# Performance work log

Hardware: AMD Instinct MI355X
Metric: run time of the kernel (lower is better)

## Reference

```python
import jax, jax.numpy as jnp
import numpy as np

EPS = 1e-8


def setup_inputs() -> dict:
    key = jax.random.key(0)
    k1, k2, k3, k4 = jax.random.split(key, 4)
    N, D, P, H = 8192, 512, 128, 128
    x1 = jax.random.normal(k1, (N, D), dtype=jnp.float32)
    proj_w1 = jax.random.normal(k2, (D, D), dtype=jnp.float32) * (1.0 / np.sqrt(D))
    proj_w2 = jax.random.normal(k3, (D, P), dtype=jnp.float32) * (1.0 / np.sqrt(D))
    gc_w = jax.random.normal(k4, (D, H), dtype=jnp.float32) * (1.0 / np.sqrt(D))
    gc_b = jnp.zeros((H,), dtype=jnp.float32)
    return {"x1": x1, "proj_w1": proj_w1, "proj_w2": proj_w2, "gc_w": gc_w, "gc_b": gc_b}


def _cosine_similarity(x):
    # torch.mm(x, x.T) / clamp(||x|| * ||x||.T, eps)
    w = jnp.sqrt(jnp.sum(x * x, axis=1, keepdims=True))  # [N,1]
    return (x @ x.T) / jnp.maximum(w * w.T, EPS)


def reference(x1, proj_w1, proj_w2, gc_w, gc_b):
    # projector: Linear(512,512,bias=False) -> ReLU -> Linear(512,P,bias=False)
    x_proj = jax.nn.relu(x1 @ proj_w1) @ proj_w2  # [N,P]
    # graph build is under @torch.no_grad(): dense fully-connected weighted graph
    A = jax.lax.stop_gradient(_cosine_similarity(x_proj))  # [N,N]
    N = x1.shape[0]
    # WGraphConv (DGL GraphConv w/ edge weights, norm='both'):
    # fully connected graph incl. self loops -> in_degree = N, norm = N^{-1/2} on both sides
    inv_n = jnp.asarray(1.0 / N, dtype=x1.dtype)
    h = x1 @ gc_w            # project first (D > H, cheaper)  [N,H]
    h = (A @ h) * inv_n      # weighted aggregate, symmetric degree norm
    return h + gc_b          # [N,H]
```

## Files before the change

### kernel.cpp

```cpp
#include <hip/hip_runtime.h>
#include <stdint.h>
#include <stddef.h>

typedef short s16x4 __attribute__((ext_vector_type(4)));
typedef short s16x8 __attribute__((ext_vector_type(8)));
typedef float f32x4 __attribute__((ext_vector_type(4)));

#define NN 8192
#define DD 512
#define PP 128
#define HH 128

__device__ __forceinline__ short f2bf(float f) {
  unsigned u = __builtin_bit_cast(unsigned, f);
  u = (u + 0x7fffu + ((u >> 16) & 1u)) >> 16;
  return (short)u;
}

__device__ __forceinline__ void async16(const void* g, void* l) {
  __builtin_amdgcn_global_load_lds(
      (const __attribute__((address_space(1))) unsigned int*)g,
      (__attribute__((address_space(3))) unsigned int*)l, 16, 0, 0);
}

template <int MF>
__device__ __forceinline__ void gemm_core2(
    const short* __restrict__ A, long lda,
    const short* __restrict__ BT, long ldb,
    long rowBase, long colBase, int k0, int k1,
    short* As0, short* Bs0, short* As1, short* Bs1,
    f32x4 (*acc)[4]) {
  const int tid  = threadIdx.x;
  const int lane = tid & 63;
  const int wid  = tid >> 6;
  const int wr   = (wid >> 1) * (MF * 16);
  const int wc   = (wid & 1) * 64;
  const int srow = lane >> 3;
  const int skk  = (lane & 7) * 8;

#define STAGE_(AS, BS, KK)                                                    \
  do {                                                                        \
    _Pragma("unroll")                                                         \
    for (int it = 0; it < MF; ++it) {                                         \
      int r = wid * (MF * 8) + it * 8;                                        \
      async16(A + (rowBase + r + srow) * lda + (KK) + skk, (AS) + r * 64);    \
    }                                                                         \
    _Pragma("unroll")                                                         \
    for (int it = 0; it < 4; ++it) {                                          \
      int r = wid * 32 + it * 8;                                              \
      async16(BT + (colBase + r + srow) * ldb + (KK) + skk, (BS) + r * 64);   \
    }                                                                         \
  } while (0)

  STAGE_(As0, Bs0, k0);
  __syncthreads();
  for (int k = k0; k < k1; k += 64) {
    if (k + 64 < k1) STAGE_(As1, Bs1, k + 64);
#pragma unroll
    for (int ks = 0; ks < 64; ks += 32) {
      s16x8 af[MF], bfv[4];
#pragma unroll
      for (int i = 0; i < MF; ++i)
        af[i]  = *(const s16x8*)(As0 + (wr + i * 16 + (lane & 15)) * 64 + ks + (lane >> 4) * 8);
#pragma unroll
      for (int i = 0; i < 4; ++i)
        bfv[i] = *(const s16x8*)(Bs0 + (wc + i * 16 + (lane & 15)) * 64 + ks + (lane >> 4) * 8);
#pragma unroll
      for (int mi = 0; mi < MF; ++mi)
#pragma unroll
        for (int ni = 0; ni < 4; ++ni)
          acc[mi][ni] = __builtin_amdgcn_mfma_f32_16x16x32_bf16(af[mi], bfv[ni], acc[mi][ni], 0, 0, 0);
    }
    __syncthreads();
    short* t0 = As0; As0 = As1; As1 = t0;
    short* t1 = Bs0; Bs0 = Bs1; Bs1 = t1;
  }
#undef STAGE_
}

__device__ __forceinline__ void zero_acc2(f32x4 (*acc)[4], int mf) {
  f32x4 z = {0.f, 0.f, 0.f, 0.f};
  for (int i = 0; i < mf; ++i)
    for (int j = 0; j < 4; ++j) acc[i][j] = z;
}

__global__ __launch_bounds__(256) void k_prep(
    const float* __restrict__ x1, const float* __restrict__ w1,
    const float* __restrict__ w2, const float* __restrict__ gcw,
    short* __restrict__ x1b, short* __restrict__ w1t,
    short* __restrict__ w2t, short* __restrict__ gcwt) {
  long b = blockIdx.x;
  int t = threadIdx.x;
  if (b < 4096) {
    long i = b * 256 + t;
    float4 v = ((const float4*)x1)[i];
    s16x4 o;
    o[0] = f2bf(v.x); o[1] = f2bf(v.y); o[2] = f2bf(v.z); o[3] = f2bf(v.w);
    *(s16x4*)(x1b + i * 4) = o;
  } else if (b < 4096 + 1024) {
    long i = (b - 4096) * 256 + t;
    int n = (int)(i >> 9), k = (int)(i & 511);
    w1t[i] = f2bf(w1[(long)k * DD + n]);
  } else if (b < 4096 + 1024 + 256) {
    long i = (b - 5120) * 256 + t;
    int n = (int)(i >> 9), k = (int)(i & 511);
    w2t[i] = f2bf(w2[(long)k * PP + n]);
  } else {
    long i = (b - 5376) * 256 + t;
    int n = (int)(i >> 9), k = (int)(i & 511);
    gcwt[i] = f2bf(gcw[(long)k * HH + n]);
  }
}

__global__ __launch_bounds__(256) void k_g13(const short* __restrict__ x1b,
                                             const short* __restrict__ w1t,
                                             const short* __restrict__ gcwt,
                                             short* __restrict__ Y,
                                             short* __restrict__ hT) {
  __shared__ __align__(16) char smem[49152];
  short* As0 = (short*)smem;
  short* As1 = (short*)(smem + 8192);
  short* Bs0 = (short*)(smem + 16384);
  short* Bs1 = (short*)(smem + 32768);
  f32x4 acc[2][4];
  zero_acc2(acc, 2);
  const int bx = blockIdx.x;
  const int lane = threadIdx.x & 63, wid = threadIdx.x >> 6;
  const int wr = (wid >> 1) * 32, wc = (wid & 1) * 64;
  if (bx < 512) {
    long rowBase = (long)(bx >> 2) * 64;
    long colBase = (long)(bx & 3) * 128;
    gemm_core2<2>(x1b, DD, w1t, DD, rowBase, colBase, 0, DD, As0, Bs0, As1, Bs1, acc);
#pragma unroll
    for (int mi = 0; mi < 2; ++mi)
#pragma unroll
      for (int ni = 0; ni < 4; ++ni)
#pragma unroll
        for (int r = 0; r < 4; ++r) {
          long m = rowBase + wr + mi * 16 + ((lane >> 4) << 2) + r;
          long n = colBase + wc + ni * 16 + (lane & 15);
          float v = acc[mi][ni][r];
          Y[m * DD + n] = f2bf(v > 0.f ? v : 0.f);
        }
  } else {
    long rowBase = (long)(bx - 512) * 64;
    gemm_core2<2>(x1b, DD, gcwt, DD, rowBase, 0, 0, DD, As0, Bs0, As1, Bs1, acc);
    short (*hs)[66] = (short(*)[66])smem;
#pragma unroll
    for (int mi = 0; mi < 2; ++mi)
#pragma unroll
      for (int ni = 0; ni < 4; ++ni)
#pragma unroll
        for (int r = 0; r < 4; ++r) {
          int m = wr + mi * 16 + ((lane >> 4) << 2) + r;
          int n = wc + ni * 16 + (lane & 15);
          hs[n][m] = f2bf(acc[mi][ni][r]);
        }
    __syncthreads();
    int t = threadIdx.x;
    int h = t >> 1, m0 = (t & 1) * 32;
#pragma unroll
    for (int j0 = 0; j0 < 32; j0 += 8) {
      s16x8 o;
#pragma unroll
      for (int u = 0; u < 8; ++u) o[u] = hs[h][m0 + j0 + u];
      *(s16x8*)(hT + (long)h * NN + rowBase + m0 + j0) = o;
    }
  }
}

__global__ __launch_bounds__(256) void k_g2(const short* __restrict__ Y,
                                            const short* __restrict__ w2t,
                                            short* __restrict__ xp,
                                            short* __restrict__ xpT,
                                            float* __restrict__ invnw) {
  __shared__ __align__(16) char smem[49152];
  short* As0 = (short*)smem;
  short* As1 = (short*)(smem + 8192);
  short* Bs0 = (short*)(smem + 16384);
  short* Bs1 = (short*)(smem + 32768);
  __shared__ float invw_s[64];
  f32x4 acc[2][4];
  zero_acc2(acc, 2);
  long rowBase = (long)blockIdx.x * 64;
  gemm_core2<2>(Y, DD, w2t, DD, rowBase, 0, 0, DD, As0, Bs0, As1, Bs1, acc);
  const int lane = threadIdx.x & 63, wid = threadIdx.x >> 6;
  const int wr = (wid >> 1) * 32, wc = (wid & 1) * 64;
  float (*xs)[129] = (float(*)[129])smem;
#pragma unroll
  for (int mi = 0; mi < 2; ++mi)
#pragma unroll
    for (int ni = 0; ni < 4; ++ni)
#pragma unroll
      for (int r = 0; r < 4; ++r)
        xs[wr + mi * 16 + ((lane >> 4) << 2) + r][wc + ni * 16 + (lane & 15)] = acc[mi][ni][r];
  __syncthreads();
  int t = threadIdx.x;
  if (t < 64) {
    float s = 0.f;
#pragma unroll 8
    for (int i = 0; i < 128; ++i) { int c = (t + i) & 127; float v = xs[t][c]; s += v * v; }
    float nr = sqrtf(s);
    invnw[rowBase + t] = 1.f / (8192.f * nr);
    invw_s[t] = 1.f / nr;
  }
  __syncthreads();
#pragma unroll
  for (int i = 0; i < 4; ++i) {
    int seg = i * 256 + t;
    int r = seg >> 4, c0 = (seg & 15) * 8;
    s16x8 o;
#pragma unroll
    for (int u = 0; u < 8; ++u) o[u] = f2bf(xs[r][c0 + u]);
    *(s16x8*)(xp + (long)(rowBase + r) * PP + c0) = o;
  }
  int c = t >> 1, n0 = (t & 1) * 32;
#pragma unroll
  for (int j0 = 0; j0 < 32; j0 += 8) {
    s16x8 o;
#pragma unroll
    for (int u = 0; u < 8; ++u) {
      int n = n0 + j0 + u;
      o[u] = f2bf(xs[n][c] * invw_s[n]);
    }
    *(s16x8*)(xpT + (long)c * NN + rowBase + n0 + j0) = o;
  }
}

__global__ __launch_bounds__(256) void k_ge(const short* __restrict__ xpT,
                                            const short* __restrict__ hT,
                                            float* __restrict__ Gp) {
  __shared__ __align__(16) char smem[65536];
  short* As0 = (short*)smem;
  short* As1 = (short*)(smem + 16384);
  short* Bs0 = (short*)(smem + 32768);
  short* Bs1 = (short*)(smem + 49152);
  f32x4 acc[4][4];
  zero_acc2(acc, 4);
  int s = blockIdx.x;
  gemm_core2<4>(xpT, NN, hT, NN, 0, 0, s * 128, s * 128 + 128, As0, Bs0, As1, Bs1, acc);
  const int lane = threadIdx.x & 63, wid = threadIdx.x >> 6;
  const int wr = (wid >> 1) * 64, wc = (wid & 1) * 64;
#pragma unroll
  for (int mi = 0; mi < 4; ++mi)
#pragma unroll
    for (int ni = 0; ni < 4; ++ni)
#pragma unroll
      for (int r = 0; r < 4; ++r) {
        int m = wr + mi * 16 + ((lane >> 4) << 2) + r;
        int n = wc + ni * 16 + (lane & 15);
        Gp[(long)s * (PP * HH) + m * HH + n] = acc[mi][ni][r];
      }
}

__global__ __launch_bounds__(256) void k_red(const float* __restrict__ Gp,
                                             short* __restrict__ GT) {
  int i = blockIdx.x * 256 + threadIdx.x;
  float s = 0.f;
#pragma unroll 8
  for (int j = 0; j < 64; ++j) s += Gp[j * (PP * HH) + i];
  int p = i >> 7, h = i & 127;
  GT[h * PP + p] = f2bf(s);
}

__global__ __launch_bounds__(256) void k_gf(const short* __restrict__ xp,
                                            const short* __restrict__ GT,
                                            const float* __restrict__ invnw,
                                            const float* __restrict__ gcb,
                                            float* __restrict__ out) {
  __shared__ __align__(16) char smem[49152];
  short* As0 = (short*)smem;
  short* As1 = (short*)(smem + 8192);
  short* Bs0 = (short*)(smem + 16384);
  short* Bs1 = (short*)(smem + 32768);
  f32x4 acc[2][4];
  zero_acc2(acc, 2);
  long rowBase = (long)blockIdx.x * 64;
  gemm_core2<2>(xp, PP, GT, PP, rowBase, 0, 0, PP, As0, Bs0, As1, Bs1, acc);
  const int lane = threadIdx.x & 63, wid = threadIdx.x >> 6;
  const int wr = (wid >> 1) * 32, wc = (wid & 1) * 64;
#pragma unroll
  for (int mi = 0; mi < 2; ++mi)
#pragma unroll
    for (int ni = 0; ni < 4; ++ni)
#pragma unroll
      for (int r = 0; r < 4; ++r) {
        long m = rowBase + wr + mi * 16 + ((lane >> 4) << 2) + r;
        int n = wc + ni * 16 + (lane & 15);
        out[m * HH + n] = acc[mi][ni][r] * invnw[m] + gcb[n];
      }
}

extern "C" void kernel_launch(void* const* d_in, const int* in_sizes, int n_in,
                              void* d_out, int out_size, void* d_ws, size_t ws_size,
                              hipStream_t stream) {
  const float* x1  = (const float*)d_in[0];
  const float* w1  = (const float*)d_in[1];
  const float* w2  = (const float*)d_in[2];
  const float* gcw = (const float*)d_in[3];
  const float* gcb = (const float*)d_in[4];
  float* out = (float*)d_out;

  char* ws = (char*)d_ws;
  size_t off = 0;
  auto alloc = [&](size_t bytes) -> char* {
    char* p = ws + off;
    off += (bytes + 255) & ~(size_t)255;
    return p;
  };
  short* x1b  = (short*)alloc((size_t)NN * DD * 2);
  short* w1t  = (short*)alloc((size_t)DD * DD * 2);
  short* w2t  = (short*)alloc((size_t)PP * DD * 2);
  short* gcwt = (short*)alloc((size_t)HH * DD * 2);
  short* Y    = (short*)alloc((size_t)NN * DD * 2);
  short* xp   = (short*)alloc((size_t)NN * PP * 2);
  short* xpT  = (short*)alloc((size_t)NN * PP * 2);
  short* hT   = (short*)alloc((size_t)NN * HH * 2);
  float* invnw = (float*)alloc((size_t)NN * 4);
  float* Gp   = (float*)alloc((size_t)64 * PP * HH * 4);
  short* GT   = (short*)alloc((size_t)PP * HH * 2);

  hipLaunchKernelGGL(k_prep, dim3(5632), dim3(256), 0, stream,
                     x1, w1, w2, gcw, x1b, w1t, w2t, gcwt);
  hipLaunchKernelGGL(k_g13, dim3(640), dim3(256), 0, stream, x1b, w1t, gcwt, Y, hT);
  hipLaunchKernelGGL(k_g2, dim3(128), dim3(256), 0, stream, Y, w2t, xp, xpT, invnw);
  hipLaunchKernelGGL(k_ge, dim3(64), dim3(256), 0, stream, xpT, hT, Gp);
  hipLaunchKernelGGL(k_red, dim3(64), dim3(256), 0, stream, Gp, GT);
  hipLaunchKernelGGL(k_gf, dim3(128), dim3(256), 0, stream, xp, GT, invnw, gcb, out);
}
```

Baseline: 51.77 us.

## Fuse xp^T·h partial GEMM into projector second-GEMM kernel via LDS

Merges k_g2 and k_ge into one kernel. Each 64-row block keeps its normalized transposed projection tile in LDS, loads the matching 64-column slice of hT, and computes a 128x128 partial of xp^T·h directly. This removes the xpT global round-trip and one launch. In exchange it doubles the partial buffer to 128 slices, so the reduction kernel reads twice as much data.

```diff
diff --git a/kernel.cpp b/kernel.cpp
--- a/kernel.cpp
+++ b/kernel.cpp
@@ -169,88 +169,110 @@
   }
 }
 
-__global__ __launch_bounds__(256) void k_g2(const short* __restrict__ Y,
-                                            const short* __restrict__ w2t,
-                                            short* __restrict__ xp,
-                                            short* __restrict__ xpT,
-                                            float* __restrict__ invnw) {
-  __shared__ __align__(16) char smem[49152];
+__global__ __launch_bounds__(256) void k_g2e(const short* __restrict__ Y,
+                                             const short* __restrict__ w2t,
+                                             const short* __restrict__ hT,
+                                             short* __restrict__ xp,
+                                             float* __restrict__ invnw,
+                                             float* __restrict__ Gp) {
+  __shared__ __align__(16) char smem[50176];
   short* As0 = (short*)smem;
   short* As1 = (short*)(smem + 8192);
   short* Bs0 = (short*)(smem + 16384);
   short* Bs1 = (short*)(smem + 32768);
-  __shared__ float invw_s[64];
   f32x4 acc[2][4];
   zero_acc2(acc, 2);
-  long rowBase = (long)blockIdx.x * 64;
+  const long rowBase = (long)blockIdx.x * 64;
   gemm_core2<2>(Y, DD, w2t, DD, rowBase, 0, 0, DD, As0, Bs0, As1, Bs1, acc);
-  const int lane = threadIdx.x & 63, wid = threadIdx.x >> 6;
-  const int wr = (wid >> 1) * 32, wc = (wid & 1) * 64;
-  float (*xs)[129] = (float(*)[129])smem;
-#pragma unroll
-  for (int mi = 0; mi < 2; ++mi)
-#pragma unroll
-    for (int ni = 0; ni < 4; ++ni)
-#pragma unroll
-      for (int r = 0; r < 4; ++r)
-        xs[wr + mi * 16 + ((lane >> 4) << 2) + r][wc + ni * 16 + (lane & 15)] = acc[mi][ni][r];
+  const int t = threadIdx.x;
+  const int lane = t & 63, wid = t >> 6;
+  {
+    const int wr = (wid >> 1) * 32, wc = (wid & 1) * 64;
+    float (*xs)[129] = (float(*)[129])smem;
+    float* invw_s = (float*)(smem + 49920);
+    short* xpt_s = (short*)(smem + 33536);
+#pragma unroll
+    for (int mi = 0; mi < 2; ++mi)
+#pragma unroll
+      for (int ni = 0; ni < 4; ++ni)
+#pragma unroll
+        for (int r = 0; r < 4; ++r)
+          xs[wr + mi * 16 + ((lane >> 4) << 2) + r][wc + ni * 16 + (lane & 15)] = acc[mi][ni][r];
+    __syncthreads();
+    if (t < 64) {
+      float s = 0.f;
+#pragma unroll 8
+      for (int i = 0; i < 128; ++i) { int c = (t + i) & 127; float v = xs[t][c]; s += v * v; }
+      float nr = sqrtf(s);
+      invnw[rowBase + t] = 1.f / (8192.f * nr);
+      invw_s[t] = 1.f / nr;
+    }
+    __syncthreads();
+#pragma unroll
+    for (int i = 0; i < 4; ++i) {
+      int seg = i * 256 + t;
+      int r = seg >> 4, c0 = (seg & 15) * 8;
+      s16x8 o;
+#pragma unroll
+      for (int u = 0; u < 8; ++u) o[u] = f2bf(xs[r][c0 + u]);
+      *(s16x8*)(xp + (long)(rowBase + r) * PP + c0) = o;
+    }
+    int c = t >> 1, n0 = (t & 1) * 32;
+#pragma unroll
+    for (int j0 = 0; j0 < 32; j0 += 8) {
+      s16x8 o;
+#pragma unroll
+      for (int u = 0; u < 8; ++u) {
+        int n = n0 + j0 + u;
+        o[u] = f2bf(xs[n][c] * invw_s[n]);
+      }
+      *(s16x8*)(xpt_s + c * 64 + n0 + j0) = o;
+    }
+  }
   __syncthreads();
-  int t = threadIdx.x;
-  if (t < 64) {
-    float s = 0.f;
-#pragma unroll 8
-    for (int i = 0; i < 128; ++i) { int c = (t + i) & 127; float v = xs[t][c]; s += v * v; }
-    float nr = sqrtf(s);
-    invnw[rowBase + t] = 1.f / (8192.f * nr);
-    invw_s[t] = 1.f / nr;
+  {
+    short* hts = (short*)smem;
+    const int srow = lane >> 3, skk = (lane & 7) * 8;
+#pragma unroll
+    for (int it = 0; it < 4; ++it) {
+      int r = wid * 32 + it * 8;
+      async16(hT + (long)(r + srow) * NN + rowBase + skk, hts + r * 64);
+    }
   }
   __syncthreads();
-#pragma unroll
-  for (int i = 0; i < 4; ++i) {
-    int seg = i * 256 + t;
-    int r = seg >> 4, c0 = (seg & 15) * 8;
-    s16x8 o;
-#pragma unroll
-    for (int u = 0; u < 8; ++u) o[u] = f2bf(xs[r][c0 + u]);
-    *(s16x8*)(xp + (long)(rowBase + r) * PP + c0) = o;
-  }
-  int c = t >> 1, n0 = (t & 1) * 32;
-#pragma unroll
-  for (int j0 = 0; j0 < 32; j0 += 8) {
-    s16x8 o;
-#pragma unroll
-    for (int u = 0; u < 8; ++u) {
-      int n = n0 + j0 + u;
-      o[u] = f2bf(xs[n][c] * invw_s[n]);
-    }
-    *(s16x8*)(xpT + (long)c * NN + rowBase + n0 + j0) = o;
-  }
-}
-
-__global__ __launch_bounds__(256) void k_ge(const short* __restrict__ xpT,
-                                            const short* __restrict__ hT,
-                                            float* __restrict__ Gp) {
-  __shared__ __align__(16) char smem[65536];
-  short* As0 = (short*)smem;
-  short* As1 = (short*)(smem + 16384);
-  short* Bs0 = (short*)(smem + 32768);
-  short* Bs1 = (short*)(smem + 49152);
-  f32x4 acc[4][4];
-  zero_acc2(acc, 4);
-  int s = blockIdx.x;
-  gemm_core2<4>(xpT, NN, hT, NN, 0, 0, s * 128, s * 128 + 128, As0, Bs0, As1, Bs1, acc);
-  const int lane = threadIdx.x & 63, wid = threadIdx.x >> 6;
-  const int wr = (wid >> 1) * 64, wc = (wid & 1) * 64;
-#pragma unroll
-  for (int mi = 0; mi < 4; ++mi)
-#pragma unroll
-    for (int ni = 0; ni < 4; ++ni)
-#pragma unroll
-      for (int r = 0; r < 4; ++r) {
-        int m = wr + mi * 16 + ((lane >> 4) << 2) + r;
-        int n = wc + ni * 16 + (lane & 15);
-        Gp[(long)s * (PP * HH) + m * HH + n] = acc[mi][ni][r];
-      }
+  {
+    const short* xpt_s = (const short*)(smem + 33536);
+    const short* hts = (const short*)smem;
+    const int wr = (wid >> 1) * 64, wc = (wid & 1) * 64;
+    f32x4 acc2[4][4];
+    zero_acc2(acc2, 4);
+#pragma unroll
+    for (int ks = 0; ks < 64; ks += 32) {
+      s16x8 af[4], bfv[4];
+#pragma unroll
+      for (int i = 0; i < 4; ++i)
+        af[i]  = *(const s16x8*)(xpt_s + (wr + i * 16 + (lane & 15)) * 64 + ks + (lane >> 4) * 8);
+#pragma unroll
+      for (int i = 0; i < 4; ++i)
+        bfv[i] = *(const s16x8*)(hts + (wc + i * 16 + (lane & 15)) * 64 + ks + (lane >> 4) * 8);
+#pragma unroll
+      for (int mi = 0; mi < 4; ++mi)
+#pragma unroll
+        for (int ni = 0; ni < 4; ++ni)
+          acc2[mi][ni] = __builtin_amdgcn_mfma_f32_16x16x32_bf16(af[mi], bfv[ni], acc2[mi][ni], 0, 0, 0);
+    }
+    float* gp = Gp + (long)blockIdx.x * (PP * HH);
+#pragma unroll
+    for (int mi = 0; mi < 4; ++mi)
+#pragma unroll
+      for (int ni = 0; ni < 4; ++ni)
+#pragma unroll
+        for (int r = 0; r < 4; ++r) {
+          int m = wr + mi * 16 + ((lane >> 4) << 2) + r;
+          int n = wc + ni * 16 + (lane & 15);
+          gp[m * HH + n] = acc2[mi][ni][r];
+        }
+  }
 }
 
 __global__ __launch_bounds__(256) void k_red(const float* __restrict__ Gp,
@@ -258,7 +280,7 @@
   int i = blockIdx.x * 256 + threadIdx.x;
   float s = 0.f;
 #pragma unroll 8
-  for (int j = 0; j < 64; ++j) s += Gp[j * (PP * HH) + i];
+  for (int j = 0; j < 128; ++j) s += Gp[j * (PP * HH) + i];
   int p = i >> 7, h = i & 127;
   GT[h * PP + p] = f2bf(s);
 }
@@ -314,17 +336,15 @@
   short* gcwt = (short*)alloc((size_t)HH * DD * 2);
   short* Y    = (short*)alloc((size_t)NN * DD * 2);
   short* xp   = (short*)alloc((size_t)NN * PP * 2);
-  short* xpT  = (short*)alloc((size_t)NN * PP * 2);
   short* hT   = (short*)alloc((size_t)NN * HH * 2);
   float* invnw = (float*)alloc((size_t)NN * 4);
-  float* Gp   = (float*)alloc((size_t)64 * PP * HH * 4);
+  float* Gp   = (float*)alloc((size_t)128 * PP * HH * 4);
   short* GT   = (short*)alloc((size_t)PP * HH * 2);
 
   hipLaunchKernelGGL(k_prep, dim3(5632), dim3(256), 0, stream,
                      x1, w1, w2, gcw, x1b, w1t, w2t, gcwt);
   hipLaunchKernelGGL(k_g13, dim3(640), dim3(256), 0, stream, x1b, w1t, gcwt, Y, hT);
-  hipLaunchKernelGGL(k_g2, dim3(128), dim3(256), 0, stream, Y, w2t, xp, xpT, invnw);
-  hipLaunchKernelGGL(k_ge, dim3(64), dim3(256), 0, stream, xpT, hT, Gp);
+  hipLaunchKernelGGL(k_g2e, dim3(128), dim3(256), 0, stream, Y, w2t, hT, xp, invnw, Gp);
   hipLaunchKernelGGL(k_red, dim3(64), dim3(256), 0, stream, Gp, GT);
   hipLaunchKernelGGL(k_gf, dim3(128), dim3(256), 0, stream, xp, GT, invnw, gcb, out);
 }
```

New measurement: 49.94 us. 3.5% less time.
